# Kernel tuning notes

Hardware: AMD Instinct MI355X
Metric: run time of the kernel (lower is better)

Reference implementation:

```python
import jax, jax.numpy as jnp
import numpy as np

T, H, I, E, TOP_K = 4096, 2048, 768, 16, 2


def _pack_i2s(tern):
    # tern: int8 in {-1,0,1}, shape [..., K] with K % 4 == 0
    m = (tern + 1).astype(jnp.uint8)  # map to {0,1,2}
    m = m.reshape(*tern.shape[:-1], -1, 4)
    return (m[..., 0] | (m[..., 1] << 2) | (m[..., 2] << 4) | (m[..., 3] << 6)).astype(jnp.uint8)


def _quantize_alpha(alpha):
    # per-column alpha -> int8 with global scale (quantize_alpha_int8)
    scale = jnp.maximum(jnp.abs(alpha).max(), 1e-8) / 127.0
    q = jnp.clip(jnp.round(alpha / scale), -128, 127).astype(jnp.int8)
    return q, scale.astype(jnp.float32)


def _unpack_i2s(packed, K, alpha):
    # packed: uint8 [..., N, K//4]; alpha: [..., K] per input column
    shifts = jnp.array([0, 2, 4, 6], dtype=jnp.uint8)
    ext = (packed[..., None] >> shifts) & jnp.uint8(3)  # [..., N, K//4, 4]
    vals = ext.reshape(*packed.shape[:-1], K).astype(jnp.float32) - 1.0  # {-1,0,1}
    return vals * alpha[..., None, :]


def setup_inputs() -> dict:
    key = jax.random.key(0)
    ks = jax.random.split(key, 6)
    x = jax.random.normal(ks[0], (T, H), dtype=jnp.float32)
    router_logits = jax.random.normal(ks[1], (T, E), dtype=jnp.float32)
    tern13 = jax.random.randint(ks[2], (E, 2 * I, H), -1, 2, dtype=jnp.int8)
    tern2 = jax.random.randint(ks[3], (E, H, I), -1, 2, dtype=jnp.int8)
    a13 = jax.random.uniform(ks[4], (E, H), minval=0.01, maxval=0.05, dtype=jnp.float32)
    a2 = jax.random.uniform(ks[5], (E, I), minval=0.01, maxval=0.05, dtype=jnp.float32)
    w13_alpha_q, w13_alpha_scale = _quantize_alpha(a13)
    w2_alpha_q, w2_alpha_scale = _quantize_alpha(a2)
    return {
        "x": x,
        "router_logits": router_logits,
        "w13_packed": _pack_i2s(tern13),
        "w13_alpha_q": w13_alpha_q,
        "w13_alpha_scale": w13_alpha_scale,
        "w2_packed": _pack_i2s(tern2),
        "w2_alpha_q": w2_alpha_q,
        "w2_alpha_scale": w2_alpha_scale,
    }


def reference(x, router_logits, w13_packed, w13_alpha_q, w13_alpha_scale,
              w2_packed, w2_alpha_q, w2_alpha_scale):
    # dequant int8 alphas, then dequant 2-bit ternary weights
    a13 = w13_alpha_q.astype(jnp.float32) * w13_alpha_scale  # [E, H]
    a2 = w2_alpha_q.astype(jnp.float32) * w2_alpha_scale     # [E, I]
    w13 = _unpack_i2s(w13_packed, H, a13)  # [E, 2I, H]
    w2 = _unpack_i2s(w2_packed, I, a2)     # [E, H, I]

    # top-k routing with renormalized softmax weights
    probs = jax.nn.softmax(router_logits, axis=-1)
    topw, topi = jax.lax.top_k(probs, TOP_K)           # [T, k]
    topw = topw / topw.sum(axis=-1, keepdims=True)
    combine = jnp.sum(jax.nn.one_hot(topi, E, dtype=x.dtype) * topw[..., None], axis=1)  # [T, E]

    # grouped expert matmuls (dense dispatch over experts)
    gu = jnp.einsum('th,enh->ten', x, w13)             # [T, E, 2I]
    gate, up = jnp.split(gu, 2, axis=-1)
    act = jax.nn.silu(gate) * up                       # [T, E, I]
    down = jnp.einsum('tei,ehi->teh', act, w2)         # [T, E, H]
    return jnp.einsum('te,teh->th', combine, down)     # [T, H]
```

## Files before the change

### kernel.cpp

```cpp
#include <hip/hip_runtime.h>
#include <stdint.h>

#define T_TOK 4096
#define HDIM  2048
#define IDIM  768
#define NEXP  16
#define NPAIR (T_TOK * 2)
#define PAIR_CAP (NPAIR + 256)

typedef float f32x4 __attribute__((ext_vector_type(4)));
typedef __bf16 bf16x8 __attribute__((ext_vector_type(8)));
typedef unsigned short u16x8 __attribute__((ext_vector_type(8)));
typedef unsigned int u32;
typedef u32 u32x4 __attribute__((ext_vector_type(4)));
typedef const __attribute__((address_space(1))) u32* as1_u32p;
typedef __attribute__((address_space(3))) u32* as3_u32p;

__device__ __forceinline__ unsigned short f2bf(float f) {
  u32 u = __float_as_uint(f);
  u += 0x7FFFu + ((u >> 16) & 1u);
  return (unsigned short)(u >> 16);
}

__device__ __forceinline__ f32x4 mfma16(bf16x8 a, bf16x8 b, f32x4 c) {
  return __builtin_amdgcn_mfma_f32_16x16x32_bf16(a, b, c, 0, 0, 0);
}

__device__ __forceinline__ bf16x8 expand8(u32 w, int qshift) {
  w >>= qshift;
  const u32 t0 = w & 0x03030303u;
  const u32 h0 = __builtin_amdgcn_perm(0u, 0x003F00BFu, t0);
  const u32 l0 = __builtin_amdgcn_perm(0u, 0x00800080u, t0);
  const u32 t1 = (w >> 2) & 0x03030303u;
  const u32 h1 = __builtin_amdgcn_perm(0u, 0x003F00BFu, t1);
  const u32 l1 = __builtin_amdgcn_perm(0u, 0x00800080u, t1);
  u32x4 o;
  o[0] = __builtin_amdgcn_perm(h0, l0, 0x05010400u);
  o[1] = __builtin_amdgcn_perm(h0, l0, 0x07030602u);
  o[2] = __builtin_amdgcn_perm(h1, l1, 0x05010400u);
  o[3] = __builtin_amdgcn_perm(h1, l1, 0x07030602u);
  return __builtin_bit_cast(bf16x8, o);
}

__global__ __launch_bounds__(256) void route_kernel(
    const float* __restrict__ logits, int* __restrict__ counts,
    int* __restrict__ t2i, float* __restrict__ t2w) {
  const int t = blockIdx.x * 256 + threadIdx.x;
  if (t >= T_TOK) return;
  const float* l = logits + t * NEXP;
  float m0 = -1e30f, m1 = -1e30f;
  int i0 = 0, i1 = 0;
#pragma unroll
  for (int j = 0; j < NEXP; ++j) {
    const float v = l[j];
    if (v > m0) { m1 = m0; i1 = i0; m0 = v; i0 = j; }
    else if (v > m1) { m1 = v; i1 = j; }
  }
  const float w0 = 1.0f / (1.0f + expf(m1 - m0));
  t2i[t] = i0 | (i1 << 8);
  t2w[t] = w0;
  atomicAdd(&counts[i0], 1);
  atomicAdd(&counts[i1], 1);
}

__global__ __launch_bounds__(256) void fill_kernel(
    const int* __restrict__ counts, const int* __restrict__ t2i,
    const float* __restrict__ t2w, int* __restrict__ cursor,
    int* __restrict__ offs, float* __restrict__ pair_wt,
    int* __restrict__ t2p0, int* __restrict__ t2p1) {
  const int t = blockIdx.x * 256 + threadIdx.x;
  if (t >= T_TOK) return;
  const int ii = t2i[t];
  const int i0 = ii & 255, i1 = (ii >> 8) & 255;
  int o0 = 0, o1 = 0;
#pragma unroll
  for (int j = 0; j < NEXP; ++j) {
    const int c = counts[j];
    o0 += (j < i0) ? c : 0;
    o1 += (j < i1) ? c : 0;
  }
  if (t == 0) {
    int run = 0;
#pragma unroll
    for (int j = 0; j < NEXP; ++j) { offs[j] = run; run += counts[j]; }
    offs[NEXP] = run;
  }
  const float w0 = t2w[t];
  const int p0 = o0 + atomicAdd(&cursor[i0], 1);
  pair_wt[p0] = w0;
  t2p0[t] = p0;
  const int p1 = o1 + atomicAdd(&cursor[i1], 1);
  pair_wt[p1] = 1.0f - w0;
  t2p1[t] = p1;
}

#define RP13_BLOCKS 3072
#define RP2_BLOCKS  1536
__global__ __launch_bounds__(256) void repack_kernel(
    const int* __restrict__ w13, u32* __restrict__ o13,
    const int* __restrict__ w2, u32* __restrict__ o2) {
  const int gid = blockIdx.x;
  const int* w;
  u32* o;
  int b;
  if (gid < RP13_BLOCKS) { w = w13; o = o13; b = gid; }
  else                   { w = w2;  o = o2;  b = gid - RP13_BLOCKS; }
  const int j0 = (b * 256 + threadIdx.x) * 4;
  const int4* w4 = (const int4*)w;
  uint4 r;
#pragma unroll
  for (int k = 0; k < 4; ++k) {
    const int4 a = w4[j0 + k];
    u32 x = (u32)(a.x & 255) | ((u32)(a.y & 255) << 8) |
            ((u32)(a.z & 255) << 16) | ((u32)(a.w & 255) << 24);
    u32 t = (x ^ (x >> 12)) & 0x0000F0F0u; x ^= t ^ (t << 12);
    t = (x ^ (x >> 6)) & 0x00CC00CCu;      x ^= t ^ (t << 6);
    ((u32*)&r)[k] = x;
  }
  ((uint4*)o)[b * 256 + threadIdx.x] = r;
}

__global__ __launch_bounds__(256) void xg_kernel(
    const float* __restrict__ x, const int* __restrict__ a13q,
    const float* __restrict__ s13p, const int* __restrict__ t2i,
    const int* __restrict__ t2p0, const int* __restrict__ t2p1,
    unsigned short* __restrict__ xg) {
  const int t = blockIdx.x;
  const int ii = t2i[t];
  const int e0 = ii & 255, e1 = (ii >> 8) & 255;
  const int p0 = t2p0[t], p1 = t2p1[t];
  const float s13 = *s13p;
  const int h0 = threadIdx.x * 8;
  const float* xp = x + (size_t)t * HDIM + h0;
  const float4 x0 = ((const float4*)xp)[0];
  const float4 x1 = ((const float4*)xp)[1];
  const int* ap0 = a13q + (size_t)e0 * HDIM + h0;
  const int* ap1 = a13q + (size_t)e1 * HDIM + h0;
  const int4 a00 = ((const int4*)ap0)[0];
  const int4 a01 = ((const int4*)ap0)[1];
  const int4 a10 = ((const int4*)ap1)[0];
  const int4 a11 = ((const int4*)ap1)[1];
  u16x8 q0, q1;
  q0[0] = f2bf(x0.x * (float)a00.x * s13);
  q0[1] = f2bf(x0.y * (float)a00.y * s13);
  q0[2] = f2bf(x0.z * (float)a00.z * s13);
  q0[3] = f2bf(x0.w * (float)a00.w * s13);
  q0[4] = f2bf(x1.x * (float)a01.x * s13);
  q0[5] = f2bf(x1.y * (float)a01.y * s13);
  q0[6] = f2bf(x1.z * (float)a01.z * s13);
  q0[7] = f2bf(x1.w * (float)a01.w * s13);
  q1[0] = f2bf(x0.x * (float)a10.x * s13);
  q1[1] = f2bf(x0.y * (float)a10.y * s13);
  q1[2] = f2bf(x0.z * (float)a10.z * s13);
  q1[3] = f2bf(x0.w * (float)a10.w * s13);
  q1[4] = f2bf(x1.x * (float)a11.x * s13);
  q1[5] = f2bf(x1.y * (float)a11.y * s13);
  q1[6] = f2bf(x1.z * (float)a11.z * s13);
  q1[7] = f2bf(x1.w * (float)a11.w * s13);
  *(u16x8*)(xg + (size_t)p0 * HDIM + h0) = q0;
  *(u16x8*)(xg + (size_t)p1 * HDIM + h0) = q1;
}

#define DMA_A(src, pitch, dst0, dst1, sidx)                                          \
  {                                                                                  \
    _Pragma("unroll") for (int c = 0; c < 2; ++c) {                                  \
      const unsigned short* gp =                                                     \
          src + (arow0 + wave * 32 + c * 16 + arow) * (pitch) + (sidx) * 64 + acol;  \
      unsigned short* lp = dst0 + (wave * 32 + c * 16) * 32;                         \
      __builtin_amdgcn_global_load_lds((as1_u32p)(const void*)gp,                    \
                                       (as3_u32p)(void*)lp, 16, 0, 0);               \
    }                                                                                \
    _Pragma("unroll") for (int c = 0; c < 2; ++c) {                                  \
      const unsigned short* gp =                                                     \
          src + (arow0 + wave * 32 + c * 16 + arow) * (pitch) + (sidx) * 64 + 32 +   \
          acol;                                                                      \
      unsigned short* lp = dst1 + (wave * 32 + c * 16) * 32;                         \
      __builtin_amdgcn_global_load_lds((as1_u32p)(const void*)gp,                    \
                                       (as3_u32p)(void*)lp, 16, 0, 0);               \
    }                                                                                \
  }

#define DMA_B1(dstq, sidx)                                                           \
  if (wave < 2) {                                                                    \
    const u32* gq = wq13 + ((size_t)e * (2 * IDIM) + wave * IDIM + nT * 64 + lane) * \
                               (HDIM / 16) + (size_t)(sidx) * 4;                     \
    u32* lp = (dstq) + wave * 256;                                                   \
    __builtin_amdgcn_global_load_lds((as1_u32p)(const void*)gq,                      \
                                     (as3_u32p)(void*)lp, 16, 0, 0);                 \
  }

#define DMA_B2(dstq, sidx)                                                           \
  if (wave < 2) {                                                                    \
    const u32* gq = wq2 + ((size_t)e * HDIM + nT * 128 + wave * 64 + lane) *         \
                              (IDIM / 16) + (size_t)(sidx) * 4;                      \
    u32* lp = (dstq) + wave * 256;                                                   \
    __builtin_amdgcn_global_load_lds((as1_u32p)(const void*)gq,                      \
                                     (as3_u32p)(void*)lp, 16, 0, 0);                 \
  }

#define G1_HALF(sAp, sBp, h)                                                        \
  {                                                                                 \
    bf16x8 af[4];                                                                   \
    _Pragma("unroll") for (int mi = 0; mi < 4; ++mi)                                \
        af[mi] = *(const bf16x8*)((sAp) + (wm * 64 + mi * 16 + ln) * 32 + quad * 8);\
    const u32 c0 = (sBp)[(wn * 32 + ln) * 4 + 2 * (h) + qsel];                      \
    const u32 c1 = (sBp)[(wn * 32 + 16 + ln) * 4 + 2 * (h) + qsel];                 \
    const u32 c2 = (sBp)[(64 + wn * 32 + ln) * 4 + 2 * (h) + qsel];                 \
    const u32 c3 = (sBp)[(64 + wn * 32 + 16 + ln) * 4 + 2 * (h) + qsel];            \
    const bf16x8 b0 = expand8(c0, qshift), b1 = expand8(c1, qshift);                \
    const bf16x8 b2 = expand8(c2, qshift), b3 = expand8(c3, qshift);                \
    _Pragma("unroll") for (int mi = 0; mi < 4; ++mi) {                              \
      acc[mi][0] = mfma16(af[mi], b0, acc[mi][0]);                                  \
      acc[mi][1] = mfma16(af[mi], b1, acc[mi][1]);                                  \
      acc[mi][2] = mfma16(af[mi], b2, acc[mi][2]);                                  \
      acc[mi][3] = mfma16(af[mi], b3, acc[mi][3]);                                  \
    }                                                                               \
  }

#define G2_HALF(sAp, sBp, h)                                                        \
  {                                                                                 \
    bf16x8 af[4];                                                                   \
    _Pragma("unroll") for (int mi = 0; mi < 4; ++mi)                                \
        af[mi] = *(const bf16x8*)((sAp) + (wm * 64 + mi * 16 + ln) * 32 + quad * 8);\
    const u32 c0 = (sBp)[(wn * 64 + ln) * 4 + 2 * (h) + qsel];                      \
    const u32 c1 = (sBp)[(wn * 64 + 16 + ln) * 4 + 2 * (h) + qsel];                 \
    const u32 c2 = (sBp)[(wn * 64 + 32 + ln) * 4 + 2 * (h) + qsel];                 \
    const u32 c3 = (sBp)[(wn * 64 + 48 + ln) * 4 + 2 * (h) + qsel];                 \
    const bf16x8 b0 = expand8(c0, qshift), b1 = expand8(c1, qshift);                \
    const bf16x8 b2 = expand8(c2, qshift), b3 = expand8(c3, qshift);                \
    _Pragma("unroll") for (int mi = 0; mi < 4; ++mi) {                              \
      acc[mi][0] = mfma16(af[mi], b0, acc[mi][0]);                                  \
      acc[mi][1] = mfma16(af[mi], b1, acc[mi][1]);                                  \
      acc[mi][2] = mfma16(af[mi], b2, acc[mi][2]);                                  \
      acc[mi][3] = mfma16(af[mi], b3, acc[mi][3]);                                  \
    }                                                                               \
  }

__global__ __launch_bounds__(256, 4) void gemm1_kernel(
    const u32* __restrict__ wq13, const int* __restrict__ a2q,
    const float* __restrict__ s2p, const int* __restrict__ counts,
    const int* __restrict__ offs, const float* __restrict__ pair_wt,
    const unsigned short* __restrict__ xg, unsigned short* __restrict__ act) {
  const int id = blockIdx.x;
  const int xcd = id & 7, sblk = id >> 3;
  const int nT = sblk % 12;
  const int gg = (sblk / 12) * 8 + xcd;
  const int e = gg & 15, mT = gg >> 4;
  const int cnt = counts[e];
  if (mT * 128 >= cnt) return;
  const int base = offs[e];
  const int tid = threadIdx.x;

  __shared__ __align__(16) unsigned short sA[2][2][128 * 32];
  __shared__ __align__(16) u32 sBq[2][512];

  const int wave = tid >> 6, lane = tid & 63;
  const int wm = wave >> 1, wn = wave & 1;
  const int quad = lane >> 4, ln = lane & 15;
  const int qsel = quad >> 1;
  const int qshift = (quad & 1) * 4;

  const int arow = lane >> 2;
  const int acol = (lane & 3) * 8;
  const size_t arow0 = (size_t)(base + mT * 128);

  f32x4 acc[4][4] = {};

  DMA_A(xg, HDIM, sA[0][0], sA[0][1], 0);
  DMA_B1(sBq[0], 0);

  const int NT = HDIM / 64;
  for (int j2 = 0; j2 < NT / 2; ++j2) {
    const int j = 2 * j2;
    __syncthreads();
    DMA_A(xg, HDIM, sA[1][0], sA[1][1], j + 1);
    DMA_B1(sBq[1], j + 1);
    __builtin_amdgcn_s_setprio(1);
    G1_HALF(sA[0][0], sBq[0], 0);
    G1_HALF(sA[0][1], sBq[0], 1);
    __builtin_amdgcn_s_setprio(0);
    __syncthreads();
    if (j2 + 1 < NT / 2) {
      DMA_A(xg, HDIM, sA[0][0], sA[0][1], j + 2);
      DMA_B1(sBq[0], j + 2);
    }
    __builtin_amdgcn_s_setprio(1);
    G1_HALF(sA[1][0], sBq[1], 0);
    G1_HALF(sA[1][1], sBq[1], 1);
    __builtin_amdgcn_s_setprio(0);
  }

  const float s2v = *s2p;
#pragma unroll
  for (int gi = 0; gi < 2; ++gi) {
    const int i = nT * 64 + wn * 32 + gi * 16 + ln;
    const float a2v = (float)a2q[e * IDIM + i] * s2v;
#pragma unroll
    for (int mi = 0; mi < 4; ++mi) {
      const f32x4 g = acc[mi][gi];
      const f32x4 u = acc[mi][gi + 2];
#pragma unroll
      for (int r = 0; r < 4; ++r) {
        const int m = mT * 128 + wm * 64 + mi * 16 + quad * 4 + r;
        if (m < cnt) {
          const float wt = pair_wt[base + m];
          const float gv = g[r];
          const float av = gv / (1.0f + __expf(-gv)) * u[r] * a2v * wt;
          act[(size_t)(base + m) * IDIM + i] = f2bf(av);
        }
      }
    }
  }
}

__global__ __launch_bounds__(256, 4) void gemm2_kernel(
    const u32* __restrict__ wq2, const int* __restrict__ counts,
    const int* __restrict__ offs, const unsigned short* __restrict__ act,
    unsigned short* __restrict__ down) {
  const int id = blockIdx.x;
  const int xcd = id & 7, sblk = id >> 3;
  const int nT = sblk & 15;
  const int gg = (sblk >> 4) * 8 + xcd;
  const int e = gg & 15, mT = gg >> 4;
  const int cnt = counts[e];
  if (mT * 128 >= cnt) return;
  const int base = offs[e];
  const int tid = threadIdx.x;

  __shared__ __align__(16) unsigned short sA[2][2][128 * 32];
  __shared__ __align__(16) u32 sBq[2][512];

  const int wave = tid >> 6, lane = tid & 63;
  const int wm = wave >> 1, wn = wave & 1;
  const int quad = lane >> 4, ln = lane & 15;
  const int qsel = quad >> 1;
  const int qshift = (quad & 1) * 4;

  const int arow = lane >> 2;
  const int acol = (lane & 3) * 8;
  const size_t arow0 = (size_t)(base + mT * 128);

  f32x4 acc[4][4] = {};

  DMA_A(act, IDIM, sA[0][0], sA[0][1], 0);
  DMA_B2(sBq[0], 0);

  const int NT = IDIM / 64;
  for (int j2 = 0; j2 < NT / 2; ++j2) {
    const int j = 2 * j2;
    __syncthreads();
    DMA_A(act, IDIM, sA[1][0], sA[1][1], j + 1);
    DMA_B2(sBq[1], j + 1);
    __builtin_amdgcn_s_setprio(1);
    G2_HALF(sA[0][0], sBq[0], 0);
    G2_HALF(sA[0][1], sBq[0], 1);
    __builtin_amdgcn_s_setprio(0);
    __syncthreads();
    if (j2 + 1 < NT / 2) {
      DMA_A(act, IDIM, sA[0][0], sA[0][1], j + 2);
      DMA_B2(sBq[0], j + 2);
    }
    __builtin_amdgcn_s_setprio(1);
    G2_HALF(sA[1][0], sBq[1], 0);
    G2_HALF(sA[1][1], sBq[1], 1);
    __builtin_amdgcn_s_setprio(0);
  }

#pragma unroll
  for (int mi = 0; mi < 4; ++mi) {
#pragma unroll
    for (int r = 0; r < 4; ++r) {
      const int ml = wm * 64 + mi * 16 + quad * 4 + r;
      const int m = mT * 128 + ml;
      if (m < cnt) {
        unsigned short* drow = down + (size_t)(base + m) * HDIM + nT * 128 + wn * 64;
#pragma unroll
        for (int ni = 0; ni < 4; ++ni)
          drow[ni * 16 + ln] = f2bf(acc[mi][ni][r]);
      }
    }
  }
}

__global__ __launch_bounds__(256) void combine_kernel(
    const int* __restrict__ t2p0, const int* __restrict__ t2p1,
    const unsigned short* __restrict__ down, float* __restrict__ out) {
  const int t = blockIdx.x;
  const int h = threadIdx.x * 8;
  const u16x8 a = *(const u16x8*)(down + (size_t)t2p0[t] * HDIM + h);
  const u16x8 b = *(const u16x8*)(down + (size_t)t2p1[t] * HDIM + h);
  f32x4 o0, o1;
#pragma unroll
  for (int j = 0; j < 4; ++j) {
    o0[j] = __uint_as_float((u32)a[j] << 16) + __uint_as_float((u32)b[j] << 16);
    o1[j] = __uint_as_float((u32)a[j + 4] << 16) + __uint_as_float((u32)b[j + 4] << 16);
  }
  float* o = out + (size_t)t * HDIM + h;
  *(f32x4*)(o) = o0;
  *(f32x4*)(o + 4) = o1;
}

extern "C" void kernel_launch(void* const* d_in, const int* in_sizes, int n_in,
                              void* d_out, int out_size, void* d_ws, size_t ws_size,
                              hipStream_t stream) {
  const float* x      = (const float*)d_in[0];
  const float* logits = (const float*)d_in[1];
  const int*   w13p   = (const int*)d_in[2];
  const int*   a13q   = (const int*)d_in[3];
  const float* s13    = (const float*)d_in[4];
  const int*   w2p    = (const int*)d_in[5];
  const int*   a2q    = (const int*)d_in[6];
  const float* s2     = (const float*)d_in[7];
  float* out = (float*)d_out;

  char* ws = (char*)d_ws;
  int*   counts     = (int*)(ws + 0);
  int*   cursor     = (int*)(ws + 64);
  int*   offs       = (int*)(ws + 128);
  int*   t2i        = (int*)(ws + 256);
  float* t2w        = (float*)(ws + 256 + 4 * T_TOK);
  int*   t2p0       = (int*)(ws + 256 + 8 * T_TOK);
  int*   t2p1       = (int*)(ws + 256 + 12 * T_TOK);
  float* pair_wt    = (float*)(ws + 256 + 16 * T_TOK);
  const size_t hdr_end = ((size_t)(256 + 16 * T_TOK + 4 * PAIR_CAP) + 255) & ~(size_t)255;

  const size_t n32_13 = (size_t)NEXP * 2 * IDIM * (HDIM / 16);
  const size_t n32_2  = (size_t)NEXP * HDIM * (IDIM / 16);
  const size_t rp13_b = n32_13 * 4, rp2_b = n32_2 * 4;
  const size_t xg_b   = (size_t)PAIR_CAP * HDIM * 2;

  u32* rp13 = (u32*)(ws + hdr_end);
  u32* rp2  = (u32*)(ws + hdr_end + rp13_b);
  unsigned short* xg  = (unsigned short*)(ws + hdr_end + rp13_b + rp2_b);
  unsigned short* act = (unsigned short*)(ws + hdr_end + rp13_b + rp2_b + xg_b);
  unsigned short* down = xg;

  hipMemsetAsync(counts, 0, 256, stream);
  route_kernel<<<T_TOK / 256, 256, 0, stream>>>(logits, counts, t2i, t2w);
  fill_kernel<<<T_TOK / 256, 256, 0, stream>>>(counts, t2i, t2w, cursor, offs,
                                               pair_wt, t2p0, t2p1);
  repack_kernel<<<RP13_BLOCKS + RP2_BLOCKS, 256, 0, stream>>>(w13p, rp13, w2p, rp2);
  xg_kernel<<<T_TOK, 256, 0, stream>>>(x, a13q, s13, t2i, t2p0, t2p1, xg);

  gemm1_kernel<<<6144, 256, 0, stream>>>(rp13, a2q, s2, counts, offs, pair_wt, xg, act);
  gemm2_kernel<<<8192, 256, 0, stream>>>(rp2, counts, offs, act, down);
  combine_kernel<<<T_TOK, 256, 0, stream>>>(t2p0, t2p1, down, out);
}
```

Before: 328.6 us.

## Replace LDS-staged GEMM tiles with direct register loads from global memory

Both expert GEMM kernels drop the shared-memory double buffer filled by global_load_lds and its __syncthreads barriers. Each wave now loads its A fragments and packed ternary B words straight from global memory into registers, double-buffered in registers. Occupancy is pinned at three waves per EU. This removes LDS traffic and block barriers, but gives up data sharing across waves: A rows are reloaded by each wn wave and B by each wm wave, which raises global/L2 traffic and makes the loop more sensitive to load latency.

```diff
diff --git a/kernel.cpp b/kernel.cpp
--- a/kernel.cpp
+++ b/kernel.cpp
@@ -13,8 +13,6 @@
 typedef unsigned short u16x8 __attribute__((ext_vector_type(8)));
 typedef unsigned int u32;
 typedef u32 u32x4 __attribute__((ext_vector_type(4)));
-typedef const __attribute__((address_space(1))) u32* as1_u32p;
-typedef __attribute__((address_space(3))) u32* as3_u32p;
 
 __device__ __forceinline__ unsigned short f2bf(float f) {
   u32 u = __float_as_uint(f);
@@ -161,82 +159,27 @@
   *(u16x8*)(xg + (size_t)p1 * HDIM + h0) = q1;
 }
 
-#define DMA_A(src, pitch, dst0, dst1, sidx)                                          \
-  {                                                                                  \
-    _Pragma("unroll") for (int c = 0; c < 2; ++c) {                                  \
-      const unsigned short* gp =                                                     \
-          src + (arow0 + wave * 32 + c * 16 + arow) * (pitch) + (sidx) * 64 + acol;  \
-      unsigned short* lp = dst0 + (wave * 32 + c * 16) * 32;                         \
-      __builtin_amdgcn_global_load_lds((as1_u32p)(const void*)gp,                    \
-                                       (as3_u32p)(void*)lp, 16, 0, 0);               \
-    }                                                                                \
-    _Pragma("unroll") for (int c = 0; c < 2; ++c) {                                  \
-      const unsigned short* gp =                                                     \
-          src + (arow0 + wave * 32 + c * 16 + arow) * (pitch) + (sidx) * 64 + 32 +   \
-          acol;                                                                      \
-      unsigned short* lp = dst1 + (wave * 32 + c * 16) * 32;                         \
-      __builtin_amdgcn_global_load_lds((as1_u32p)(const void*)gp,                    \
-                                       (as3_u32p)(void*)lp, 16, 0, 0);               \
-    }                                                                                \
-  }
-
-#define DMA_B1(dstq, sidx)                                                           \
-  if (wave < 2) {                                                                    \
-    const u32* gq = wq13 + ((size_t)e * (2 * IDIM) + wave * IDIM + nT * 64 + lane) * \
-                               (HDIM / 16) + (size_t)(sidx) * 4;                     \
-    u32* lp = (dstq) + wave * 256;                                                   \
-    __builtin_amdgcn_global_load_lds((as1_u32p)(const void*)gq,                      \
-                                     (as3_u32p)(void*)lp, 16, 0, 0);                 \
-  }
-
-#define DMA_B2(dstq, sidx)                                                           \
-  if (wave < 2) {                                                                    \
-    const u32* gq = wq2 + ((size_t)e * HDIM + nT * 128 + wave * 64 + lane) *         \
-                              (IDIM / 16) + (size_t)(sidx) * 4;                      \
-    u32* lp = (dstq) + wave * 256;                                                   \
-    __builtin_amdgcn_global_load_lds((as1_u32p)(const void*)gq,                      \
-                                     (as3_u32p)(void*)lp, 16, 0, 0);                 \
-  }
-
-#define G1_HALF(sAp, sBp, h)                                                        \
-  {                                                                                 \
-    bf16x8 af[4];                                                                   \
-    _Pragma("unroll") for (int mi = 0; mi < 4; ++mi)                                \
-        af[mi] = *(const bf16x8*)((sAp) + (wm * 64 + mi * 16 + ln) * 32 + quad * 8);\
-    const u32 c0 = (sBp)[(wn * 32 + ln) * 4 + 2 * (h) + qsel];                      \
-    const u32 c1 = (sBp)[(wn * 32 + 16 + ln) * 4 + 2 * (h) + qsel];                 \
-    const u32 c2 = (sBp)[(64 + wn * 32 + ln) * 4 + 2 * (h) + qsel];                 \
-    const u32 c3 = (sBp)[(64 + wn * 32 + 16 + ln) * 4 + 2 * (h) + qsel];            \
-    const bf16x8 b0 = expand8(c0, qshift), b1 = expand8(c1, qshift);                \
-    const bf16x8 b2 = expand8(c2, qshift), b3 = expand8(c3, qshift);                \
-    _Pragma("unroll") for (int mi = 0; mi < 4; ++mi) {                              \
-      acc[mi][0] = mfma16(af[mi], b0, acc[mi][0]);                                  \
-      acc[mi][1] = mfma16(af[mi], b1, acc[mi][1]);                                  \
-      acc[mi][2] = mfma16(af[mi], b2, acc[mi][2]);                                  \
-      acc[mi][3] = mfma16(af[mi], b3, acc[mi][3]);                                  \
-    }                                                                               \
-  }
-
-#define G2_HALF(sAp, sBp, h)                                                        \
-  {                                                                                 \
-    bf16x8 af[4];                                                                   \
-    _Pragma("unroll") for (int mi = 0; mi < 4; ++mi)                                \
-        af[mi] = *(const bf16x8*)((sAp) + (wm * 64 + mi * 16 + ln) * 32 + quad * 8);\
-    const u32 c0 = (sBp)[(wn * 64 + ln) * 4 + 2 * (h) + qsel];                      \
-    const u32 c1 = (sBp)[(wn * 64 + 16 + ln) * 4 + 2 * (h) + qsel];                 \
-    const u32 c2 = (sBp)[(wn * 64 + 32 + ln) * 4 + 2 * (h) + qsel];                 \
-    const u32 c3 = (sBp)[(wn * 64 + 48 + ln) * 4 + 2 * (h) + qsel];                 \
-    const bf16x8 b0 = expand8(c0, qshift), b1 = expand8(c1, qshift);                \
-    const bf16x8 b2 = expand8(c2, qshift), b3 = expand8(c3, qshift);                \
-    _Pragma("unroll") for (int mi = 0; mi < 4; ++mi) {                              \
-      acc[mi][0] = mfma16(af[mi], b0, acc[mi][0]);                                  \
-      acc[mi][1] = mfma16(af[mi], b1, acc[mi][1]);                                  \
-      acc[mi][2] = mfma16(af[mi], b2, acc[mi][2]);                                  \
-      acc[mi][3] = mfma16(af[mi], b3, acc[mi][3]);                                  \
-    }                                                                               \
-  }
-
-__global__ __launch_bounds__(256, 4) void gemm1_kernel(
+#define LDA(dst, h)                                                     \
+  _Pragma("unroll") for (int mi = 0; mi < 4; ++mi)                      \
+      dst[mi] = *(const bf16x8*)(ap + (size_t)mi * 16 * APITCH + (h) * 32);
+#define LDB(dst, h)                                                     \
+  dst[0] = bp0[(h) * 2]; dst[1] = bp1[(h) * 2];                         \
+  dst[2] = bp2[(h) * 2]; dst[3] = bp3[(h) * 2];
+#define FMA4(A, BC)                                                     \
+  {                                                                     \
+    const bf16x8 b0 = expand8(BC[0], qshift), b1 = expand8(BC[1], qshift); \
+    const bf16x8 b2 = expand8(BC[2], qshift), b3 = expand8(BC[3], qshift); \
+    _Pragma("unroll") for (int mi = 0; mi < 4; ++mi) {                  \
+      acc[mi][0] = mfma16(A[mi], b0, acc[mi][0]);                       \
+      acc[mi][1] = mfma16(A[mi], b1, acc[mi][1]);                       \
+      acc[mi][2] = mfma16(A[mi], b2, acc[mi][2]);                       \
+      acc[mi][3] = mfma16(A[mi], b3, acc[mi][3]);                       \
+    }                                                                   \
+  }
+
+#define APITCH HDIM
+__attribute__((amdgpu_waves_per_eu(3, 3))) __global__ __launch_bounds__(256)
+void gemm1_kernel(
     const u32* __restrict__ wq13, const int* __restrict__ a2q,
     const float* __restrict__ s2p, const int* __restrict__ counts,
     const int* __restrict__ offs, const float* __restrict__ pair_wt,
@@ -251,43 +194,36 @@
   const int base = offs[e];
   const int tid = threadIdx.x;
 
-  __shared__ __align__(16) unsigned short sA[2][2][128 * 32];
-  __shared__ __align__(16) u32 sBq[2][512];
-
   const int wave = tid >> 6, lane = tid & 63;
   const int wm = wave >> 1, wn = wave & 1;
   const int quad = lane >> 4, ln = lane & 15;
   const int qsel = quad >> 1;
   const int qshift = (quad & 1) * 4;
 
-  const int arow = lane >> 2;
-  const int acol = (lane & 3) * 8;
   const size_t arow0 = (size_t)(base + mT * 128);
+  const unsigned short* ap = xg + (arow0 + wm * 64 + ln) * (size_t)HDIM + quad * 8;
+
+  const u32* bp0 = wq13 + ((size_t)e * (2 * IDIM) + nT * 64 + wn * 32 + ln) * 128 + qsel;
+  const u32* bp1 = bp0 + (size_t)16 * 128;
+  const u32* bp2 = bp0 + (size_t)IDIM * 128;
+  const u32* bp3 = bp2 + (size_t)16 * 128;
 
   f32x4 acc[4][4] = {};
-
-  DMA_A(xg, HDIM, sA[0][0], sA[0][1], 0);
-  DMA_B1(sBq[0], 0);
-
-  const int NT = HDIM / 64;
-  for (int j2 = 0; j2 < NT / 2; ++j2) {
-    const int j = 2 * j2;
-    __syncthreads();
-    DMA_A(xg, HDIM, sA[1][0], sA[1][1], j + 1);
-    DMA_B1(sBq[1], j + 1);
-    __builtin_amdgcn_s_setprio(1);
-    G1_HALF(sA[0][0], sBq[0], 0);
-    G1_HALF(sA[0][1], sBq[0], 1);
-    __builtin_amdgcn_s_setprio(0);
-    __syncthreads();
-    if (j2 + 1 < NT / 2) {
-      DMA_A(xg, HDIM, sA[0][0], sA[0][1], j + 2);
-      DMA_B1(sBq[0], j + 2);
+  bf16x8 A0[4], A1[4];
+  u32 B0[4], B1[4];
+
+  LDA(A0, 0);
+  LDB(B0, 0);
+  const int NH = HDIM / 32;
+  for (int j = 0; j < NH; j += 2) {
+    LDA(A1, j + 1);
+    LDB(B1, j + 1);
+    FMA4(A0, B0);
+    if (j + 2 < NH) {
+      LDA(A0, j + 2);
+      LDB(B0, j + 2);
     }
-    __builtin_amdgcn_s_setprio(1);
-    G1_HALF(sA[1][0], sBq[1], 0);
-    G1_HALF(sA[1][1], sBq[1], 1);
-    __builtin_amdgcn_s_setprio(0);
+    FMA4(A1, B1);
   }
 
   const float s2v = *s2p;
@@ -312,8 +248,11 @@
     }
   }
 }
-
-__global__ __launch_bounds__(256, 4) void gemm2_kernel(
+#undef APITCH
+
+#define APITCH IDIM
+__attribute__((amdgpu_waves_per_eu(3, 3))) __global__ __launch_bounds__(256)
+void gemm2_kernel(
     const u32* __restrict__ wq2, const int* __restrict__ counts,
     const int* __restrict__ offs, const unsigned short* __restrict__ act,
     unsigned short* __restrict__ down) {
@@ -327,43 +266,36 @@
   const int base = offs[e];
   const int tid = threadIdx.x;
 
-  __shared__ __align__(16) unsigned short sA[2][2][128 * 32];
-  __shared__ __align__(16) u32 sBq[2][512];
-
   const int wave = tid >> 6, lane = tid & 63;
   const int wm = wave >> 1, wn = wave & 1;
   const int quad = lane >> 4, ln = lane & 15;
   const int qsel = quad >> 1;
   const int qshift = (quad & 1) * 4;
 
-  const int arow = lane >> 2;
-  const int acol = (lane & 3) * 8;
   const size_t arow0 = (size_t)(base + mT * 128);
+  const unsigned short* ap = act + (arow0 + wm * 64 + ln) * (size_t)IDIM + quad * 8;
+
+  const u32* bp0 = wq2 + ((size_t)e * HDIM + nT * 128 + wn * 64 + ln) * 48 + qsel;
+  const u32* bp1 = bp0 + (size_t)16 * 48;
+  const u32* bp2 = bp0 + (size_t)32 * 48;
+  const u32* bp3 = bp0 + (size_t)48 * 48;
 
   f32x4 acc[4][4] = {};
-
-  DMA_A(act, IDIM, sA[0][0], sA[0][1], 0);
-  DMA_B2(sBq[0], 0);
-
-  const int NT = IDIM / 64;
-  for (int j2 = 0; j2 < NT / 2; ++j2) {
-    const int j = 2 * j2;
-    __syncthreads();
-    DMA_A(act, IDIM, sA[1][0], sA[1][1], j + 1);
-    DMA_B2(sBq[1], j + 1);
-    __builtin_amdgcn_s_setprio(1);
-    G2_HALF(sA[0][0], sBq[0], 0);
-    G2_HALF(sA[0][1], sBq[0], 1);
-    __builtin_amdgcn_s_setprio(0);
-    __syncthreads();
-    if (j2 + 1 < NT / 2) {
-      DMA_A(act, IDIM, sA[0][0], sA[0][1], j + 2);
-      DMA_B2(sBq[0], j + 2);
+  bf16x8 A0[4], A1[4];
+  u32 B0[4], B1[4];
+
+  LDA(A0, 0);
+  LDB(B0, 0);
+  const int NH = IDIM / 32;
+  for (int j = 0; j < NH; j += 2) {
+    LDA(A1, j + 1);
+    LDB(B1, j + 1);
+    FMA4(A0, B0);
+    if (j + 2 < NH) {
+      LDA(A0, j + 2);
+      LDB(B0, j + 2);
     }
-    __builtin_amdgcn_s_setprio(1);
-    G2_HALF(sA[1][0], sBq[1], 0);
-    G2_HALF(sA[1][1], sBq[1], 1);
-    __builtin_amdgcn_s_setprio(0);
+    FMA4(A1, B1);
   }
 
 #pragma unroll
@@ -381,6 +313,7 @@
     }
   }
 }
+#undef APITCH
 
 __global__ __launch_bounds__(256) void combine_kernel(
     const int* __restrict__ t2p0, const int* __restrict__ t2p1,
```

Result: slower. 557.8 us (+69.8%).
